# Kernel optimization log

Hardware: AMD Instinct MI355X
Metric: run time of the kernel (lower is better)

## Reference

```python
import jax, jax.numpy as jnp
import numpy as np

N, E, IN_DIM, OUT_DIM, T = 100000, 1600000, 128, 64, 8
V_THRESHOLD = 1.0
EPS = 1e-7

# ---- Lorentz manifold (curvature -1), time coordinate first ----

def _linner(a, b):
    # Lorentzian inner product <a,b>_L = -a0*b0 + sum_i ai*bi
    return -a[..., 0] * b[..., 0] + jnp.sum(a[..., 1:] * b[..., 1:], axis=-1)

def _proju(z, u):
    # project ambient vector u to tangent space at z (<z,z>_L = -1)
    return u + _linner(z, u)[..., None] * z

def _expmap(z, u):
    un = jnp.sqrt(jnp.maximum(_linner(u, u), EPS))[..., None]
    return jnp.cosh(un) * z + jnp.sinh(un) * u / un

def _dist0(z):
    # geodesic distance to origin o=(1,0,...,0): arccosh(-<o,z>_L) = arccosh(z0)
    return jnp.arccosh(jnp.maximum(z[..., 0], 1.0 + EPS))

# ---- GCNConv (torch_geometric semantics: self-loops + symmetric norm) ----

def _gcn(x, edge_index, W, b):
    src, dst = edge_index[0], edge_index[1]
    loops = jnp.arange(N, dtype=src.dtype)
    src = jnp.concatenate([src, loops])
    dst = jnp.concatenate([dst, loops])
    deg = jax.ops.segment_sum(jnp.ones_like(dst, dtype=x.dtype), dst, num_segments=N)
    dinv = jax.lax.rsqrt(jnp.maximum(deg, 1.0))  # deg >= 1 due to self-loops
    norm = dinv[src] * dinv[dst]                 # [E+N]
    h = x @ W                                    # [N, OUT_DIM]
    out = jax.ops.segment_sum(norm[:, None] * h[src], dst, num_segments=N)
    return out + b


def setup_inputs() -> dict:
    key = jax.random.key(0)
    k1, k2, k3 = jax.random.split(key, 3)
    x = jax.random.normal(k1, (N, IN_DIM), dtype=jnp.float32)
    edge_index = jax.random.randint(k2, (2, E), 0, N, dtype=jnp.int32)
    W = jax.random.normal(k3, (IN_DIM, OUT_DIM), dtype=jnp.float32) / np.sqrt(IN_DIM)
    b = jnp.zeros((OUT_DIM,), dtype=jnp.float32)
    return {"x": x, "edge_index": edge_index, "W": W, "b": b}


def reference(x, edge_index, W, b):
    h = _gcn(x, edge_index, W, b)                       # [N, D]
    origin = jnp.zeros_like(h).at[..., 0].set(1.0)      # manifold origin
    x_seq = jnp.broadcast_to(h, (T,) + h.shape)         # [T, N, D]

    def step(z, x_t):
        u = _proju(z, x_t)                              # input current in T_z M
        z_new = _expmap(z, u)                           # charge along geodesic
        v = _dist0(z_new)                               # membrane potential [N]
        spike = v >= V_THRESHOLD
        z_out = jnp.where(spike[..., None], origin, z_new)  # hard reset
        return z_out, (spike.astype(h.dtype), z_out)

    _, (o_seq, z_seq) = jax.lax.scan(step, origin, x_seq)
    return o_seq, z_seq  # [T, N], [T, N, D]
```

## Files before the change

kernel.cpp:

```cpp
#include <hip/hip_runtime.h>
#include <math.h>

#define IN_DIM_C 128
#define OUT_DIM_C 64
#define T_STEPS 8
#define KC_MAX 512
#define PTILE 2048

__device__ __forceinline__ float4 f4zero() { return make_float4(0.f, 0.f, 0.f, 0.f); }

__global__ __launch_bounds__(256) void k_hist(const int* __restrict__ dst,
                                              int* __restrict__ chist, int E) {
    __shared__ int hh[KC_MAX];
    const int tid = threadIdx.x;
    for (int i = tid; i < KC_MAX; i += 256) hh[i] = 0;
    __syncthreads();
    long base = (long)blockIdx.x * 4096;
    #pragma unroll
    for (int j = 0; j < 16; ++j) {
        long e = base + j * 256 + tid;
        if (e < E) atomicAdd(&hh[dst[e] >> 8], 1);
    }
    __syncthreads();
    for (int i = tid; i < KC_MAX; i += 256)
        if (hh[i]) atomicAdd(&chist[i], hh[i]);
}

__global__ __launch_bounds__(64) void k_scanK(const int* __restrict__ chist,
                                              int* __restrict__ gcursor,
                                              int* __restrict__ offsets,
                                              int kc, int n, int E) {
    int lane = threadIdx.x;
    int carry = 0;
    for (int c = 0; c * 64 < kc; ++c) {
        int idx = c * 64 + lane;
        int v = (idx < kc) ? chist[idx] : 0;
        int x = v;
        #pragma unroll
        for (int off = 1; off < 64; off <<= 1) {
            int t = __shfl_up(x, off, 64);
            if (lane >= off) x += t;
        }
        if (idx < kc) gcursor[idx] = carry + x - v;
        carry += __shfl(x, 63, 64);
    }
    if (lane == 0) offsets[n] = E;
}

__global__ __launch_bounds__(256) void k_gemm(const float* __restrict__ x,
                                              const float* __restrict__ W,
                                              float* __restrict__ h,
                                              int n, int n_groups) {
    __shared__ __align__(16) float Ws[IN_DIM_C * OUT_DIM_C];
    __shared__ __align__(16) float xs[16 * 136];

    for (int i = threadIdx.x; i < IN_DIM_C * OUT_DIM_C / 4; i += 256)
        ((float4*)Ws)[i] = ((const float4*)W)[i];

    const int ln = threadIdx.x >> 4;
    const int dg = threadIdx.x & 15;
    const float4* Ws4 = (const float4*)Ws;

    for (int g = blockIdx.x; g < n_groups; g += gridDim.x) {
        int node_base = g * 16;
        __syncthreads();
        for (int f = threadIdx.x; f < 512; f += 256) {
            int row = f >> 5, c4 = f & 31;
            int node = node_base + row;
            float4 v = f4zero();
            if (node < n) v = *(const float4*)&x[(long)node * IN_DIM_C + c4 * 4];
            *(float4*)&xs[row * 136 + c4 * 4] = v;
        }
        __syncthreads();

        int node = node_base + ln;
        float4 acc = f4zero();
        #pragma unroll
        for (int k = 0; k < IN_DIM_C; k += 4) {
            float4 xv = *(const float4*)&xs[ln * 136 + k];
            float4 w0 = Ws4[(k + 0) * 16 + dg];
            float4 w1 = Ws4[(k + 1) * 16 + dg];
            float4 w2 = Ws4[(k + 2) * 16 + dg];
            float4 w3 = Ws4[(k + 3) * 16 + dg];
            acc.x = fmaf(xv.x, w0.x, acc.x); acc.y = fmaf(xv.x, w0.y, acc.y);
            acc.z = fmaf(xv.x, w0.z, acc.z); acc.w = fmaf(xv.x, w0.w, acc.w);
            acc.x = fmaf(xv.y, w1.x, acc.x); acc.y = fmaf(xv.y, w1.y, acc.y);
            acc.z = fmaf(xv.y, w1.z, acc.z); acc.w = fmaf(xv.y, w1.w, acc.w);
            acc.x = fmaf(xv.z, w2.x, acc.x); acc.y = fmaf(xv.z, w2.y, acc.y);
            acc.z = fmaf(xv.z, w2.z, acc.z); acc.w = fmaf(xv.z, w2.w, acc.w);
            acc.x = fmaf(xv.w, w3.x, acc.x); acc.y = fmaf(xv.w, w3.y, acc.y);
            acc.z = fmaf(xv.w, w3.z, acc.z); acc.w = fmaf(xv.w, w3.w, acc.w);
        }
        if (node < n)
            *(float4*)&h[(long)node * OUT_DIM_C + dg * 4] = acc;
    }
}

__global__ __launch_bounds__(256) void k_part(const int* __restrict__ src,
                                              const int* __restrict__ dst,
                                              int* __restrict__ gcursor,
                                              int* __restrict__ part, int E, int kc) {
    __shared__ int hist[KC_MAX];
    __shared__ int offs[KC_MAX];
    __shared__ int cur[KC_MAX];
    __shared__ int gbase[KC_MAX];
    const int tid = threadIdx.x;
    long base = (long)blockIdx.x * PTILE;

    for (int i = tid; i < KC_MAX; i += 256) hist[i] = 0;
    __syncthreads();
    #pragma unroll
    for (int j = 0; j < PTILE / 256; ++j) {
        long e = base + j * 256 + tid;
        if (e < E) atomicAdd(&hist[dst[e] >> 8], 1);
    }
    __syncthreads();
    if (tid < 64) {
        int carry = 0;
        for (int c = 0; c * 64 < kc; ++c) {
            int idx = c * 64 + tid;
            int v = (idx < kc) ? hist[idx] : 0;
            int x = v;
            #pragma unroll
            for (int off = 1; off < 64; off <<= 1) {
                int t = __shfl_up(x, off, 64);
                if (tid >= off) x += t;
            }
            if (idx < kc) { offs[idx] = carry + x - v; cur[idx] = carry + x - v; }
            carry += __shfl(x, 63, 64);
        }
    }
    __syncthreads();
    for (int b = tid; b < kc; b += 256)
        gbase[b] = hist[b] ? atomicAdd(&gcursor[b], hist[b]) : 0;
    __syncthreads();
    #pragma unroll
    for (int j = 0; j < PTILE / 256; ++j) {
        long e = base + j * 256 + tid;
        if (e < E) {
            int d = dst[e];
            int b = d >> 8;
            int r = atomicAdd(&cur[b], 1);
            part[gbase[b] + r - offs[b]] = (src[e] << 8) | (d & 255);
        }
    }
}

__global__ __launch_bounds__(256) void k_sort(const int* __restrict__ part,
                                              const int* __restrict__ gcursor,
                                              int* __restrict__ part2,
                                              int* __restrict__ offsets,
                                              float* __restrict__ dinv, int n) {
    __shared__ int cnt[256];
    __shared__ int cur[256];
    __shared__ int wsum[4], woff[4];
    const int tid = threadIdx.x;
    const int bkt = blockIdx.x;
    int start = bkt ? gcursor[bkt - 1] : 0;
    int end = gcursor[bkt];

    cnt[tid] = 0;
    __syncthreads();
    for (int i = start + tid; i < end; i += 256)
        atomicAdd(&cnt[part[i] & 255], 1);
    __syncthreads();

    int v = cnt[tid];
    int lane = tid & 63, wv = tid >> 6;
    int x = v;
    #pragma unroll
    for (int off = 1; off < 64; off <<= 1) {
        int t = __shfl_up(x, off, 64);
        if (lane >= off) x += t;
    }
    if (lane == 63) wsum[wv] = x;
    __syncthreads();
    if (tid == 0) { int c = 0; for (int w = 0; w < 4; ++w) { woff[w] = c; c += wsum[w]; } }
    __syncthreads();
    int myloc = woff[wv] + x - v;
    cur[tid] = myloc;
    int node = (bkt << 8) + tid;
    if (node < n) {
        offsets[node] = start + myloc;
        dinv[node] = rsqrtf((float)(v + 1));
    }
    __syncthreads();

    for (int i = start + tid; i < end; i += 256) {
        int p = part[i];
        int r = atomicAdd(&cur[p & 255], 1);
        part2[start + r] = ((unsigned)p) >> 8;
    }
}

__global__ __launch_bounds__(256) void k_pullspike(const int* __restrict__ offsets,
                                                   const int* __restrict__ part2,
                                                   const float* __restrict__ dinv,
                                                   const float* __restrict__ h,
                                                   const float* __restrict__ b,
                                                   float* __restrict__ o_seq,
                                                   float* __restrict__ z_seq, int n) {
    int node = (blockIdx.x * 256 + threadIdx.x) >> 6;
    int lane = threadIdx.x & 63;
    if (node >= n) return;

    int o0 = offsets[node], o1 = offsets[node + 1];
    float dd = dinv[node];
    float g = fmaf(dd * dd, h[(long)node * OUT_DIM_C + lane], b[lane]);
    int i = o0;
    for (; i + 8 <= o1; i += 8) {
        int s[8]; float nr[8], hv[8];
        #pragma unroll
        for (int k = 0; k < 8; ++k) s[k] = part2[i + k];
        #pragma unroll
        for (int k = 0; k < 8; ++k) hv[k] = h[(long)s[k] * OUT_DIM_C + lane];
        #pragma unroll
        for (int k = 0; k < 8; ++k) nr[k] = dinv[s[k]] * dd;
        #pragma unroll
        for (int k = 0; k < 8; ++k) g = fmaf(nr[k], hv[k], g);
    }
    for (; i < o1; ++i) {
        int s = part2[i];
        g = fmaf(dinv[s] * dd, h[(long)s * OUT_DIM_C + lane], g);
    }

    const float s0 = (lane == 0) ? -1.0f : 1.0f;
    const float zo = (lane == 0) ? 1.0f : 0.0f;

    auto step = [&](float z, float& zn, bool& sp) {
        float p = s0 * z * g;
        p += __shfl_xor(p, 1, 64);  p += __shfl_xor(p, 2, 64);
        p += __shfl_xor(p, 4, 64);  p += __shfl_xor(p, 8, 64);
        p += __shfl_xor(p, 16, 64); p += __shfl_xor(p, 32, 64);
        float u = fmaf(p, z, g);
        float q = s0 * u * u;
        q += __shfl_xor(q, 1, 64);  q += __shfl_xor(q, 2, 64);
        q += __shfl_xor(q, 4, 64);  q += __shfl_xor(q, 8, 64);
        q += __shfl_xor(q, 16, 64); q += __shfl_xor(q, 32, 64);
        float un = sqrtf(fmaxf(q, 1e-7f));
        float c = coshf(un);
        float sh = sinhf(un) / un;
        zn = fmaf(c, z, sh * u);
        float z0 = __shfl(zn, 0, 64);
        float v = acoshf(fmaxf(z0, 1.0f + 1e-7f));
        sp = (v >= 1.0f);
    };

    float z1; bool sp0;
    step(zo, z1, sp0);
    float r0 = sp0 ? zo : z1;

    float z = zo;
    bool at0 = true;
    for (int t = 0; t < T_STEPS; ++t) {
        float zn; bool sp;
        if (at0) { sp = sp0; zn = r0; }
        else {
            step(z, zn, sp);
            if (sp) zn = zo;
        }
        z_seq[(long)t * n * OUT_DIM_C + (long)node * OUT_DIM_C + lane] = zn;
        if (lane == 0) o_seq[(long)t * n + node] = sp ? 1.0f : 0.0f;
        z = zn;
        at0 = sp;
    }
}

__global__ __launch_bounds__(256) void k_pull(const int* __restrict__ offsets,
                                              const int* __restrict__ part2,
                                              const float* __restrict__ dinv,
                                              const float* __restrict__ h,
                                              const float* __restrict__ b,
                                              float* __restrict__ agg, int n) {
    int node = (blockIdx.x * 256 + threadIdx.x) >> 6;
    int lane = threadIdx.x & 63;
    if (node >= n) return;
    int o0 = offsets[node], o1 = offsets[node + 1];
    float dd = dinv[node];
    float acc = fmaf(dd * dd, h[(long)node * OUT_DIM_C + lane], b[lane]);
    int i = o0;
    for (; i + 8 <= o1; i += 8) {
        int s[8]; float hv[8];
        #pragma unroll
        for (int k = 0; k < 8; ++k) s[k] = part2[i + k];
        #pragma unroll
        for (int k = 0; k < 8; ++k) hv[k] = h[(long)s[k] * OUT_DIM_C + lane];
        #pragma unroll
        for (int k = 0; k < 8; ++k) acc = fmaf(dinv[s[k]] * dd, hv[k], acc);
    }
    for (; i < o1; ++i) {
        int s = part2[i];
        acc = fmaf(dinv[s] * dd, h[(long)s * OUT_DIM_C + lane], acc);
    }
    agg[(long)node * OUT_DIM_C + lane] = acc;
}

__global__ __launch_bounds__(256) void k_spike(const float* agg,
                                               float* o_seq, float* z_seq, int n) {
    int node = (blockIdx.x * 256 + threadIdx.x) >> 6;
    int lane = threadIdx.x & 63;
    if (node >= n) return;
    float g = agg[(long)node * OUT_DIM_C + lane];
    const float s0 = (lane == 0) ? -1.0f : 1.0f;
    const float zo = (lane == 0) ? 1.0f : 0.0f;

    auto step = [&](float z, float& zn, bool& sp) {
        float p = s0 * z * g;
        p += __shfl_xor(p, 1, 64);  p += __shfl_xor(p, 2, 64);
        p += __shfl_xor(p, 4, 64);  p += __shfl_xor(p, 8, 64);
        p += __shfl_xor(p, 16, 64); p += __shfl_xor(p, 32, 64);
        float u = fmaf(p, z, g);
        float q = s0 * u * u;
        q += __shfl_xor(q, 1, 64);  q += __shfl_xor(q, 2, 64);
        q += __shfl_xor(q, 4, 64);  q += __shfl_xor(q, 8, 64);
        q += __shfl_xor(q, 16, 64); q += __shfl_xor(q, 32, 64);
        float un = sqrtf(fmaxf(q, 1e-7f));
        float c = coshf(un);
        float sh = sinhf(un) / un;
        zn = fmaf(c, z, sh * u);
        float z0 = __shfl(zn, 0, 64);
        float v = acoshf(fmaxf(z0, 1.0f + 1e-7f));
        sp = (v >= 1.0f);
    };

    float z1; bool sp0;
    step(zo, z1, sp0);
    float r0 = sp0 ? zo : z1;

    float z = zo;
    bool at0 = true;
    for (int t = 0; t < T_STEPS; ++t) {
        float zn; bool sp;
        if (at0) { sp = sp0; zn = r0; }
        else {
            step(z, zn, sp);
            if (sp) zn = zo;
        }
        z_seq[(long)t * n * OUT_DIM_C + (long)node * OUT_DIM_C + lane] = zn;
        if (lane == 0) o_seq[(long)t * n + node] = sp ? 1.0f : 0.0f;
        z = zn;
        at0 = sp;
    }
}

extern "C" void kernel_launch(void* const* d_in, const int* in_sizes, int n_in,
                              void* d_out, int out_size, void* d_ws, size_t ws_size,
                              hipStream_t stream) {
    const float* x  = (const float*)d_in[0];
    const int*   ei = (const int*)d_in[1];
    const float* W  = (const float*)d_in[2];
    const float* b  = (const float*)d_in[3];
    const int N = in_sizes[0] / IN_DIM_C;
    const int E = in_sizes[1] / 2;
    const int KC = (N + 255) >> 8;

    float* out   = (float*)d_out;
    float* o_seq = out;
    float* z_seq = out + (long)T_STEPS * N;

    const int* srcp = ei;
    const int* dstp = ei + E;

    const long n_h = (long)N * OUT_DIM_C;
    const long n_meta = 2L * KC_MAX + (N + 1) + N;
    const size_t need = (size_t)(n_h + 2L * E + n_meta) * 4;

    float *h; int *part, *part2, *chist, *gcursor, *offsets; float *dinv;
    bool fused = (ws_size >= need);
    if (fused) {
        h       = (float*)d_ws;
        part    = (int*)(h + n_h);
        part2   = part + E;
        chist   = part2 + E;
    } else {
        h       = z_seq + 1L * n_h;
        part    = (int*)(z_seq + 2L * n_h);
        part2   = (int*)(z_seq + 3L * n_h);
        chist   = (int*)(z_seq + 4L * n_h);
    }
    gcursor = chist + KC_MAX;
    offsets = gcursor + KC_MAX;
    dinv    = (float*)(offsets + N + 1);

    hipMemsetAsync(chist, 0, (size_t)KC_MAX * sizeof(int), stream);
    k_hist<<<(E + 4095) / 4096, 256, 0, stream>>>(dstp, chist, E);
    k_scanK<<<1, 64, 0, stream>>>(chist, gcursor, offsets, KC, N, E);

    int n_groups = (N + 15) / 16;
    k_gemm<<<1024, 256, 0, stream>>>(x, W, h, N, n_groups);

    k_part<<<(E + PTILE - 1) / PTILE, 256, 0, stream>>>(srcp, dstp, gcursor, part, E, KC);
    k_sort<<<KC, 256, 0, stream>>>(part, gcursor, part2, offsets, dinv, N);

    if (fused) {
        k_pullspike<<<(N * 64 + 255) / 256, 256, 0, stream>>>(offsets, part2, dinv, h, b,
                                                              o_seq, z_seq, N);
    } else {
        float* agg = z_seq;
        k_pull<<<(N * 64 + 255) / 256, 256, 0, stream>>>(offsets, part2, dinv, h, b, agg, N);
        k_spike<<<(N * 64 + 255) / 256, 256, 0, stream>>>(agg, o_seq, z_seq, N);
    }
}
```

Before: 444.6 us.

## Retile GEMM for register reuse, widen sort blocks, warp-cooperative neighbor index loads

The GEMM now gives each block 64 nodes and each thread 4 nodes by 4 outputs, reusing every loaded W element across four rows. The grid-stride loop is gone and the x tile is staged once, which costs a larger shared-memory footprint. The histogram, partition and sort kernels get more blocks or wider blocks, so more threads work on the atomics and the scatter. In the fused pull-spike kernel, each lane loads one neighbour index and its dinv value, and these are broadcast with shuffles instead of every lane reloading them. The unfused fallback pull loop is simplified to a plain scalar loop.

```diff
diff --git a/kernel.cpp b/kernel.cpp
--- a/kernel.cpp
+++ b/kernel.cpp
@@ -9,15 +9,20 @@
 
 __device__ __forceinline__ float4 f4zero() { return make_float4(0.f, 0.f, 0.f, 0.f); }
 
+__device__ __forceinline__ void fma4(float4& a, float xv, const float4 w) {
+    a.x = fmaf(xv, w.x, a.x); a.y = fmaf(xv, w.y, a.y);
+    a.z = fmaf(xv, w.z, a.z); a.w = fmaf(xv, w.w, a.w);
+}
+
 __global__ __launch_bounds__(256) void k_hist(const int* __restrict__ dst,
                                               int* __restrict__ chist, int E) {
     __shared__ int hh[KC_MAX];
     const int tid = threadIdx.x;
     for (int i = tid; i < KC_MAX; i += 256) hh[i] = 0;
     __syncthreads();
-    long base = (long)blockIdx.x * 4096;
-    #pragma unroll
-    for (int j = 0; j < 16; ++j) {
+    long base = (long)blockIdx.x * 1024;
+    #pragma unroll
+    for (int j = 0; j < 4; ++j) {
         long e = base + j * 256 + tid;
         if (e < E) atomicAdd(&hh[dst[e] >> 8], 1);
     }
@@ -49,54 +54,61 @@
 
 __global__ __launch_bounds__(256) void k_gemm(const float* __restrict__ x,
                                               const float* __restrict__ W,
-                                              float* __restrict__ h,
-                                              int n, int n_groups) {
+                                              float* __restrict__ h, int n) {
     __shared__ __align__(16) float Ws[IN_DIM_C * OUT_DIM_C];
-    __shared__ __align__(16) float xs[16 * 136];
-
-    for (int i = threadIdx.x; i < IN_DIM_C * OUT_DIM_C / 4; i += 256)
-        ((float4*)Ws)[i] = ((const float4*)W)[i];
-
-    const int ln = threadIdx.x >> 4;
-    const int dg = threadIdx.x & 15;
+    __shared__ __align__(16) float xs[64 * IN_DIM_C];
+
+    const int tid = threadIdx.x;
+    const int node_base = blockIdx.x * 64;
+    const float4* x4 = (const float4*)x;
+    float4* xs4w = (float4*)xs;
+
+    #pragma unroll
+    for (int i = 0; i < 8; ++i)
+        ((float4*)Ws)[tid + i * 256] = ((const float4*)W)[tid + i * 256];
+    #pragma unroll
+    for (int i = 0; i < 8; ++i) {
+        int idx = tid + i * 256;
+        int row = idx >> 5, c4 = idx & 31;
+        int node = node_base + row;
+        xs4w[idx] = (node < n) ? x4[(long)node * 32 + c4] : f4zero();
+    }
+    __syncthreads();
+
+    const int ng = tid >> 4;
+    const int dg = tid & 15;
     const float4* Ws4 = (const float4*)Ws;
-
-    for (int g = blockIdx.x; g < n_groups; g += gridDim.x) {
-        int node_base = g * 16;
-        __syncthreads();
-        for (int f = threadIdx.x; f < 512; f += 256) {
-            int row = f >> 5, c4 = f & 31;
-            int node = node_base + row;
-            float4 v = f4zero();
-            if (node < n) v = *(const float4*)&x[(long)node * IN_DIM_C + c4 * 4];
-            *(float4*)&xs[row * 136 + c4 * 4] = v;
-        }
-        __syncthreads();
-
-        int node = node_base + ln;
-        float4 acc = f4zero();
-        #pragma unroll
-        for (int k = 0; k < IN_DIM_C; k += 4) {
-            float4 xv = *(const float4*)&xs[ln * 136 + k];
-            float4 w0 = Ws4[(k + 0) * 16 + dg];
-            float4 w1 = Ws4[(k + 1) * 16 + dg];
-            float4 w2 = Ws4[(k + 2) * 16 + dg];
-            float4 w3 = Ws4[(k + 3) * 16 + dg];
-            acc.x = fmaf(xv.x, w0.x, acc.x); acc.y = fmaf(xv.x, w0.y, acc.y);
-            acc.z = fmaf(xv.x, w0.z, acc.z); acc.w = fmaf(xv.x, w0.w, acc.w);
-            acc.x = fmaf(xv.y, w1.x, acc.x); acc.y = fmaf(xv.y, w1.y, acc.y);
-            acc.z = fmaf(xv.y, w1.z, acc.z); acc.w = fmaf(xv.y, w1.w, acc.w);
-            acc.x = fmaf(xv.z, w2.x, acc.x); acc.y = fmaf(xv.z, w2.y, acc.y);
-            acc.z = fmaf(xv.z, w2.z, acc.z); acc.w = fmaf(xv.z, w2.w, acc.w);
-            acc.x = fmaf(xv.w, w3.x, acc.x); acc.y = fmaf(xv.w, w3.y, acc.y);
-            acc.z = fmaf(xv.w, w3.z, acc.z); acc.w = fmaf(xv.w, w3.w, acc.w);
-        }
-        if (node < n)
-            *(float4*)&h[(long)node * OUT_DIM_C + dg * 4] = acc;
-    }
-}
-
-__global__ __launch_bounds__(256) void k_part(const int* __restrict__ src,
+    const float4* xs4 = (const float4*)xs;
+
+    float4 acc[4] = {f4zero(), f4zero(), f4zero(), f4zero()};
+    #pragma unroll
+    for (int c = 0; c < 32; ++c) {
+        float4 xv0 = xs4[(ng * 4 + 0) * 32 + c];
+        float4 xv1 = xs4[(ng * 4 + 1) * 32 + c];
+        float4 xv2 = xs4[(ng * 4 + 2) * 32 + c];
+        float4 xv3 = xs4[(ng * 4 + 3) * 32 + c];
+        float4 w0 = Ws4[(c * 4 + 0) * 16 + dg];
+        float4 w1 = Ws4[(c * 4 + 1) * 16 + dg];
+        float4 w2 = Ws4[(c * 4 + 2) * 16 + dg];
+        float4 w3 = Ws4[(c * 4 + 3) * 16 + dg];
+        fma4(acc[0], xv0.x, w0); fma4(acc[0], xv0.y, w1);
+        fma4(acc[0], xv0.z, w2); fma4(acc[0], xv0.w, w3);
+        fma4(acc[1], xv1.x, w0); fma4(acc[1], xv1.y, w1);
+        fma4(acc[1], xv1.z, w2); fma4(acc[1], xv1.w, w3);
+        fma4(acc[2], xv2.x, w0); fma4(acc[2], xv2.y, w1);
+        fma4(acc[2], xv2.z, w2); fma4(acc[2], xv2.w, w3);
+        fma4(acc[3], xv3.x, w0); fma4(acc[3], xv3.y, w1);
+        fma4(acc[3], xv3.z, w2); fma4(acc[3], xv3.w, w3);
+    }
+    float4* h4 = (float4*)h;
+    #pragma unroll
+    for (int j = 0; j < 4; ++j) {
+        int node = node_base + ng * 4 + j;
+        if (node < n) h4[(long)node * 16 + dg] = acc[j];
+    }
+}
+
+__global__ __launch_bounds__(512) void k_part(const int* __restrict__ src,
                                               const int* __restrict__ dst,
                                               int* __restrict__ gcursor,
                                               int* __restrict__ part, int E, int kc) {
@@ -107,11 +119,11 @@
     const int tid = threadIdx.x;
     long base = (long)blockIdx.x * PTILE;
 
-    for (int i = tid; i < KC_MAX; i += 256) hist[i] = 0;
-    __syncthreads();
-    #pragma unroll
-    for (int j = 0; j < PTILE / 256; ++j) {
-        long e = base + j * 256 + tid;
+    for (int i = tid; i < KC_MAX; i += 512) hist[i] = 0;
+    __syncthreads();
+    #pragma unroll
+    for (int j = 0; j < PTILE / 512; ++j) {
+        long e = base + j * 512 + tid;
         if (e < E) atomicAdd(&hist[dst[e] >> 8], 1);
     }
     __syncthreads();
@@ -131,12 +143,12 @@
         }
     }
     __syncthreads();
-    for (int b = tid; b < kc; b += 256)
+    for (int b = tid; b < kc; b += 512)
         gbase[b] = hist[b] ? atomicAdd(&gcursor[b], hist[b]) : 0;
     __syncthreads();
     #pragma unroll
-    for (int j = 0; j < PTILE / 256; ++j) {
-        long e = base + j * 256 + tid;
+    for (int j = 0; j < PTILE / 512; ++j) {
+        long e = base + j * 512 + tid;
         if (e < E) {
             int d = dst[e];
             int b = d >> 8;
@@ -146,11 +158,11 @@
     }
 }
 
-__global__ __launch_bounds__(256) void k_sort(const int* __restrict__ part,
-                                              const int* __restrict__ gcursor,
-                                              int* __restrict__ part2,
-                                              int* __restrict__ offsets,
-                                              float* __restrict__ dinv, int n) {
+__global__ __launch_bounds__(1024) void k_sort(const int* __restrict__ part,
+                                               const int* __restrict__ gcursor,
+                                               int* __restrict__ part2,
+                                               int* __restrict__ offsets,
+                                               float* __restrict__ dinv, int n) {
     __shared__ int cnt[256];
     __shared__ int cur[256];
     __shared__ int wsum[4], woff[4];
@@ -159,13 +171,13 @@
     int start = bkt ? gcursor[bkt - 1] : 0;
     int end = gcursor[bkt];
 
-    cnt[tid] = 0;
-    __syncthreads();
-    for (int i = start + tid; i < end; i += 256)
+    if (tid < 256) cnt[tid] = 0;
+    __syncthreads();
+    for (int i = start + tid; i < end; i += 1024)
         atomicAdd(&cnt[part[i] & 255], 1);
     __syncthreads();
 
-    int v = cnt[tid];
+    int v = (tid < 256) ? cnt[tid] : 0;
     int lane = tid & 63, wv = tid >> 6;
     int x = v;
     #pragma unroll
@@ -173,20 +185,22 @@
         int t = __shfl_up(x, off, 64);
         if (lane >= off) x += t;
     }
-    if (lane == 63) wsum[wv] = x;
+    if (tid < 256 && lane == 63) wsum[wv] = x;
     __syncthreads();
     if (tid == 0) { int c = 0; for (int w = 0; w < 4; ++w) { woff[w] = c; c += wsum[w]; } }
     __syncthreads();
-    int myloc = woff[wv] + x - v;
-    cur[tid] = myloc;
-    int node = (bkt << 8) + tid;
-    if (node < n) {
-        offsets[node] = start + myloc;
-        dinv[node] = rsqrtf((float)(v + 1));
-    }
-    __syncthreads();
-
-    for (int i = start + tid; i < end; i += 256) {
+    if (tid < 256) {
+        int myloc = woff[wv] + x - v;
+        cur[tid] = myloc;
+        int node = (bkt << 8) + tid;
+        if (node < n) {
+            offsets[node] = start + myloc;
+            dinv[node] = rsqrtf((float)(v + 1));
+        }
+    }
+    __syncthreads();
+
+    for (int i = start + tid; i < end; i += 1024) {
         int p = part[i];
         int r = atomicAdd(&cur[p & 255], 1);
         part2[start + r] = ((unsigned)p) >> 8;
@@ -207,21 +221,31 @@
     int o0 = offsets[node], o1 = offsets[node + 1];
     float dd = dinv[node];
     float g = fmaf(dd * dd, h[(long)node * OUT_DIM_C + lane], b[lane]);
-    int i = o0;
-    for (; i + 8 <= o1; i += 8) {
-        int s[8]; float nr[8], hv[8];
-        #pragma unroll
-        for (int k = 0; k < 8; ++k) s[k] = part2[i + k];
-        #pragma unroll
-        for (int k = 0; k < 8; ++k) hv[k] = h[(long)s[k] * OUT_DIM_C + lane];
-        #pragma unroll
-        for (int k = 0; k < 8; ++k) nr[k] = dinv[s[k]] * dd;
-        #pragma unroll
-        for (int k = 0; k < 8; ++k) g = fmaf(nr[k], hv[k], g);
-    }
-    for (; i < o1; ++i) {
-        int s = part2[i];
-        g = fmaf(dinv[s] * dd, h[(long)s * OUT_DIM_C + lane], g);
+
+    for (int base = o0; base < o1; base += 64) {
+        int m = o1 - base; if (m > 64) m = 64;
+        int s_l = 0; float dv_l = 0.f;
+        if (base + lane < o1) {
+            s_l = part2[base + lane];
+            dv_l = dinv[s_l];
+        }
+        int k = 0;
+        for (; k + 8 <= m; k += 8) {
+            float hv[8], w[8];
+            #pragma unroll
+            for (int j = 0; j < 8; ++j) {
+                int s = __shfl(s_l, k + j, 64);
+                w[j] = __shfl(dv_l, k + j, 64);
+                hv[j] = h[(long)s * OUT_DIM_C + lane];
+            }
+            #pragma unroll
+            for (int j = 0; j < 8; ++j) g = fmaf(w[j] * dd, hv[j], g);
+        }
+        for (; k < m; ++k) {
+            int s = __shfl(s_l, k, 64);
+            float w = __shfl(dv_l, k, 64);
+            g = fmaf(w * dd, h[(long)s * OUT_DIM_C + lane], g);
+        }
     }
 
     const float s0 = (lane == 0) ? -1.0f : 1.0f;
@@ -278,17 +302,7 @@
     int o0 = offsets[node], o1 = offsets[node + 1];
     float dd = dinv[node];
     float acc = fmaf(dd * dd, h[(long)node * OUT_DIM_C + lane], b[lane]);
-    int i = o0;
-    for (; i + 8 <= o1; i += 8) {
-        int s[8]; float hv[8];
-        #pragma unroll
-        for (int k = 0; k < 8; ++k) s[k] = part2[i + k];
-        #pragma unroll
-        for (int k = 0; k < 8; ++k) hv[k] = h[(long)s[k] * OUT_DIM_C + lane];
-        #pragma unroll
-        for (int k = 0; k < 8; ++k) acc = fmaf(dinv[s[k]] * dd, hv[k], acc);
-    }
-    for (; i < o1; ++i) {
+    for (int i = o0; i < o1; ++i) {
         int s = part2[i];
         acc = fmaf(dinv[s] * dd, h[(long)s * OUT_DIM_C + lane], acc);
     }
@@ -383,14 +397,13 @@
     dinv    = (float*)(offsets + N + 1);
 
     hipMemsetAsync(chist, 0, (size_t)KC_MAX * sizeof(int), stream);
-    k_hist<<<(E + 4095) / 4096, 256, 0, stream>>>(dstp, chist, E);
+    k_hist<<<(E + 1023) / 1024, 256, 0, stream>>>(dstp, chist, E);
     k_scanK<<<1, 64, 0, stream>>>(chist, gcursor, offsets, KC, N, E);
 
-    int n_groups = (N + 15) / 16;
-    k_gemm<<<1024, 256, 0, stream>>>(x, W, h, N, n_groups);
-
-    k_part<<<(E + PTILE - 1) / PTILE, 256, 0, stream>>>(srcp, dstp, gcursor, part, E, KC);
-    k_sort<<<KC, 256, 0, stream>>>(part, gcursor, part2, offsets, dinv, N);
+    k_gemm<<<(N + 63) / 64, 256, 0, stream>>>(x, W, h, N);
+
+    k_part<<<(E + PTILE - 1) / PTILE, 512, 0, stream>>>(srcp, dstp, gcursor, part, E, KC);
+    k_sort<<<KC, 1024, 0, stream>>>(part, gcursor, part2, offsets, dinv, N);
 
     if (fused) {
         k_pullspike<<<(N * 64 + 255) / 256, 256, 0, stream>>>(offsets, part2, dinv, h, b,
```

Result: slower. 977.7 us (+119.9%).
